# Performance work log

Measured on AMD Instinct MI355X. Metric: run time of the kernel, lower is better.

The kernel has to match this reference:

```python
import jax, jax.numpy as jnp
import numpy as np

# ---- constants from init_kwargs ----
L = 10.0
N = 512
DT = 5e-05
NUM_STEPS = 256
NUM_G = 4
DX = L / (N - 1)
DX2 = DX * DX
DT2 = DT * DT


def _wave_speed_map(alpha):
    # matches create_wave_speed_map: 2 + sum_i a_i * exp(-((x-cx_i)^2 + (y-cy_i)^2))
    x = jnp.linspace(-(L // 2), L // 2, N, dtype=jnp.float32)
    X, Y = jnp.meshgrid(x, x, indexing='ij')  # (N, N)
    amps = alpha[:NUM_G]
    cx = alpha[NUM_G:2 * NUM_G]
    cy = alpha[2 * NUM_G:3 * NUM_G]
    g = jnp.exp(-((X[None] - cx[:, None, None]) ** 2 + (Y[None] - cy[:, None, None]) ** 2))  # (G,N,N)
    return 2.0 + jnp.einsum('g,gij->ij', amps, g)


def setup_inputs() -> dict:
    key = jax.random.key(0)
    k1, k2 = jax.random.split(key)
    u0 = jax.random.normal(k1, (N, N), dtype=jnp.float32)
    alpha = jax.random.uniform(k2, (4 * NUM_G,), dtype=jnp.float32)
    return {"u0": u0, "alpha": alpha}


def reference(u0, alpha):
    c2_int = _wave_speed_map(alpha)[1:-1, 1:-1] ** 2  # (N-2, N-2)

    def step(carry, _):
        u, u_prev = carry
        u_xx = (u[:-2, 1:-1] - 2.0 * u[1:-1, 1:-1] + u[2:, 1:-1]) / DX2
        u_yy = (u[1:-1, :-2] - 2.0 * u[1:-1, 1:-1] + u[1:-1, 2:]) / DX2
        interior = 2.0 * u[1:-1, 1:-1] - u_prev[1:-1, 1:-1] + DT2 * c2_int * (u_xx + u_yy)
        # boundaries are zeroed every step in the original
        u_new = jnp.zeros_like(u).at[1:-1, 1:-1].set(interior)
        return (u_new, u), u  # record state BEFORE stepping, like intermediate_steps[t] = T

    (_, _), traj = jax.lax.scan(step, (u0, u0), None, length=NUM_STEPS)
    # original returns intermediate_steps[1:]
    return traj[1:]
```

## Files before the change

### kernel.cpp

```cpp
#include <hip/hip_runtime.h>

#define GN      512
#define GNN     (GN * GN)
#define TILE    32
#define HALO    16
#define REGW    64
#define LSTR    68
#define LROWS   66
#define NTHR    1024

__global__ __launch_bounds__(NTHR)
void wave_chunk(const float* __restrict__ ucur,
                const float* __restrict__ uprev,
                const float* __restrict__ alpha,
                float* __restrict__ out,
                int slice0, int nsteps)
{
    __shared__ __align__(16) float bufA[LROWS * LSTR];
    __shared__ __align__(16) float bufB[LROWS * LSTR];

    const int tid = threadIdx.x;
    const int r   = tid >> 4;
    const int c   = tid & 15;
    const int jc  = c << 2;

    const int bx  = blockIdx.x & 15;
    const int by  = blockIdx.x >> 4;
    const int ti0 = by * TILE, tj0 = bx * TILE;
    const int gi  = ti0 - HALO + r;
    const int gj0 = tj0 - HALO + jc;

    for (int k = tid; k < LROWS * LSTR; k += NTHR) { bufA[k] = 0.0f; bufB[k] = 0.0f; }

    const float DX = 10.0f / 511.0f;
    const float K  = (5e-5f * 5e-5f) / (DX * DX);

    float amp[4], cxs[4], cys[4];
#pragma unroll
    for (int g = 0; g < 4; ++g) {
        amp[g] = alpha[g];
        cxs[g] = alpha[4 + g];
        cys[g] = alpha[8 + g];
    }
    const float X = -5.0f + (float)gi * DX;
    float4 c2v;
    {
        float cm[4];
#pragma unroll
        for (int m = 0; m < 4; ++m) {
            const float Y = -5.0f + (float)(gj0 + m) * DX;
            float cv = 2.0f;
#pragma unroll
            for (int g = 0; g < 4; ++g) {
                const float dx = X - cxs[g], dy = Y - cys[g];
                cv += amp[g] * __expf(-(dx * dx + dy * dy));
            }
            cm[m] = cv * cv;
        }
        c2v = make_float4(cm[0], cm[1], cm[2], cm[3]);
    }

    const bool rin = (gi >= 1) && (gi <= GN - 2);
    float4 bm;
    bm.x = (rin && gj0 + 0 >= 1 && gj0 + 0 <= GN - 2) ? 1.0f : 0.0f;
    bm.y = (rin && gj0 + 1 >= 1 && gj0 + 1 <= GN - 2) ? 1.0f : 0.0f;
    bm.z = (rin && gj0 + 2 >= 1 && gj0 + 2 <= GN - 2) ? 1.0f : 0.0f;
    bm.w = (rin && gj0 + 3 >= 1 && gj0 + 3 <= GN - 2) ? 1.0f : 0.0f;

    float4 cur4 = make_float4(0.f, 0.f, 0.f, 0.f);
    float4 prv4 = cur4;
    const bool rowin = ((unsigned)gi < GN);
    const bool colin = ((unsigned)gj0 <= (GN - 4));
    if (rowin && colin) {
        const size_t g = (size_t)gi * GN + gj0;
        cur4 = *reinterpret_cast<const float4*>(ucur + g);
        prv4 = *reinterpret_cast<const float4*>(uprev + g);
    }

    const int idx = (r + 1) * LSTR + jc;
    *reinterpret_cast<float4*>(bufA + idx) = cur4;
    __syncthreads();

    const bool inTile = (r >= HALO) && (r < HALO + TILE) &&
                        (jc >= HALO) && (jc < HALO + TILE);

    float* A = bufA;
    float* B = bufB;
    for (int s = 0; s < nsteps; ++s) {
        const float4 up = *reinterpret_cast<const float4*>(A + idx - LSTR);
        const float4 dn = *reinterpret_cast<const float4*>(A + idx + LSTR);
        const float  lf = A[idx - 1];
        const float  rt = A[idx + 4];

        float4 nw;
        nw.x = bm.x * (2.0f * cur4.x - prv4.x + K * c2v.x * (up.x + dn.x + lf     + cur4.y - 4.0f * cur4.x));
        nw.y = bm.y * (2.0f * cur4.y - prv4.y + K * c2v.y * (up.y + dn.y + cur4.x + cur4.z - 4.0f * cur4.y));
        nw.z = bm.z * (2.0f * cur4.z - prv4.z + K * c2v.z * (up.z + dn.z + cur4.y + cur4.w - 4.0f * cur4.z));
        nw.w = bm.w * (2.0f * cur4.w - prv4.w + K * c2v.w * (up.w + dn.w + cur4.z + rt     - 4.0f * cur4.w));

        *reinterpret_cast<float4*>(B + idx) = nw;
        prv4 = cur4;
        cur4 = nw;

        if (inTile) {
            *reinterpret_cast<float4*>(out + (size_t)(slice0 + s) * GNN
                                           + (size_t)gi * GN + gj0) = nw;
        }

        __syncthreads();
        float* t = A; A = B; B = t;
    }
}

extern "C" void kernel_launch(void* const* d_in, const int* in_sizes, int n_in,
                              void* d_out, int out_size, void* d_ws, size_t ws_size,
                              hipStream_t stream)
{
    const float* u0    = (const float*)d_in[0];
    const float* alpha = (const float*)d_in[1];
    float*       out   = (float*)d_out;

    int base = 0;
    for (int k = 0; k < 16; ++k) {
        const int steps = (k < 15) ? 16 : 15;
        const float* uc = (k == 0) ? u0 : out + (size_t)(base - 1) * GNN;
        const float* up = (k == 0) ? u0 : out + (size_t)(base - 2) * GNN;
        wave_chunk<<<dim3(256), dim3(NTHR), 0, stream>>>(uc, up, alpha, out, base, steps);
        base += steps;
    }
}
```

Before: 401.3 us.

## Exchange column neighbors via DPP wave shifts and only edge rows via LDS

Remaps each wavefront to a 4-row by 64-column strip held in registers. Left and right neighbors now come from DPP wave-shift intrinsics instead of LDS. Only the top and bottom rows of each strip are exchanged through small LDS surfaces. This cuts LDS reads and writes per step. The step loop is also unrolled by two so the register ping-pong needs no copies, and the barrier becomes an explicit lgkmcnt wait plus s_barrier. The risks are that it relies on DPP wave-shift support and zero-fill at the wave edges, and that output stores are now scalar rather than float4.

```diff
diff --git a/kernel.cpp b/kernel.cpp
--- a/kernel.cpp
+++ b/kernel.cpp
@@ -4,10 +4,17 @@
 #define GNN     (GN * GN)
 #define TILE    32
 #define HALO    16
-#define REGW    64
-#define LSTR    68
-#define LROWS   66
 #define NTHR    1024
+#define SURF    (17 * 64)
+
+__device__ __forceinline__ float dpp_left(float x) {
+    return __int_as_float(__builtin_amdgcn_update_dpp(
+        0, __float_as_int(x), 0x130, 0xF, 0xF, true));
+}
+__device__ __forceinline__ float dpp_right(float x) {
+    return __int_as_float(__builtin_amdgcn_update_dpp(
+        0, __float_as_int(x), 0x138, 0xF, 0xF, true));
+}
 
 __global__ __launch_bounds__(NTHR)
 void wave_chunk(const float* __restrict__ ucur,
@@ -16,21 +23,22 @@
                 float* __restrict__ out,
                 int slice0, int nsteps)
 {
-    __shared__ __align__(16) float bufA[LROWS * LSTR];
-    __shared__ __align__(16) float bufB[LROWS * LSTR];
+    __shared__ __align__(16) float surf[4 * SURF];
+    float* const topA = surf;
+    float* const botA = surf + SURF;
+    float* const topB = surf + 2 * SURF;
+    float* const botB = surf + 3 * SURF;
 
     const int tid = threadIdx.x;
-    const int r   = tid >> 4;
-    const int c   = tid & 15;
-    const int jc  = c << 2;
+    const int w   = tid >> 6;
+    const int l   = tid & 63;
 
     const int bx  = blockIdx.x & 15;
     const int by  = blockIdx.x >> 4;
-    const int ti0 = by * TILE, tj0 = bx * TILE;
-    const int gi  = ti0 - HALO + r;
-    const int gj0 = tj0 - HALO + jc;
+    const int gi0 = by * TILE - HALO + 4 * w;
+    const int gj  = bx * TILE - HALO + l;
 
-    for (int k = tid; k < LROWS * LSTR; k += NTHR) { bufA[k] = 0.0f; bufB[k] = 0.0f; }
+    for (int k = tid; k < 4 * SURF; k += NTHR) surf[k] = 0.0f;
 
     const float DX = 10.0f / 511.0f;
     const float K  = (5e-5f * 5e-5f) / (DX * DX);
@@ -42,74 +50,71 @@
         cxs[g] = alpha[4 + g];
         cys[g] = alpha[8 + g];
     }
-    const float X = -5.0f + (float)gi * DX;
-    float4 c2v;
-    {
-        float cm[4];
+    const float Y = -5.0f + (float)gj * DX;
+    float dy2[4];
 #pragma unroll
-        for (int m = 0; m < 4; ++m) {
-            const float Y = -5.0f + (float)(gj0 + m) * DX;
-            float cv = 2.0f;
+    for (int g = 0; g < 4; ++g) { const float dy = Y - cys[g]; dy2[g] = dy * dy; }
+
+    float kc2[4], bm[4], cur[4], prv[4];
+    const bool colin = ((unsigned)gj < GN);
 #pragma unroll
-            for (int g = 0; g < 4; ++g) {
-                const float dx = X - cxs[g], dy = Y - cys[g];
-                cv += amp[g] * __expf(-(dx * dx + dy * dy));
-            }
-            cm[m] = cv * cv;
+    for (int k = 0; k < 4; ++k) {
+        const int gi = gi0 + k;
+        const float X = -5.0f + (float)gi * DX;
+        float cv = 2.0f;
+#pragma unroll
+        for (int g = 0; g < 4; ++g) {
+            const float dx = X - cxs[g];
+            cv += amp[g] * __expf(-(dx * dx + dy2[g]));
         }
-        c2v = make_float4(cm[0], cm[1], cm[2], cm[3]);
+        kc2[k] = K * (cv * cv);
+        bm[k]  = (gi >= 1 && gi <= GN - 2 && gj >= 1 && gj <= GN - 2) ? 1.0f : 0.0f;
+        const bool inb = colin && ((unsigned)gi < GN);
+        const long off = (long)gi * GN + gj;
+        cur[k] = inb ? ucur[off] : 0.0f;
+        prv[k] = inb ? uprev[off] : 0.0f;
     }
 
-    const bool rin = (gi >= 1) && (gi <= GN - 2);
-    float4 bm;
-    bm.x = (rin && gj0 + 0 >= 1 && gj0 + 0 <= GN - 2) ? 1.0f : 0.0f;
-    bm.y = (rin && gj0 + 1 >= 1 && gj0 + 1 <= GN - 2) ? 1.0f : 0.0f;
-    bm.z = (rin && gj0 + 2 >= 1 && gj0 + 2 <= GN - 2) ? 1.0f : 0.0f;
-    bm.w = (rin && gj0 + 3 >= 1 && gj0 + 3 <= GN - 2) ? 1.0f : 0.0f;
+    const int sTop = (w << 6) + l;
+    const int sBot = sTop + 64;
 
-    float4 cur4 = make_float4(0.f, 0.f, 0.f, 0.f);
-    float4 prv4 = cur4;
-    const bool rowin = ((unsigned)gi < GN);
-    const bool colin = ((unsigned)gj0 <= (GN - 4));
-    if (rowin && colin) {
-        const size_t g = (size_t)gi * GN + gj0;
-        cur4 = *reinterpret_cast<const float4*>(ucur + g);
-        prv4 = *reinterpret_cast<const float4*>(uprev + g);
-    }
-
-    const int idx = (r + 1) * LSTR + jc;
-    *reinterpret_cast<float4*>(bufA + idx) = cur4;
+    __syncthreads();
+    topA[sTop] = cur[0];
+    botA[sBot] = cur[3];
     __syncthreads();
 
-    const bool inTile = (r >= HALO) && (r < HALO + TILE) &&
-                        (jc >= HALO) && (jc < HALO + TILE);
+    const bool inTile = (w >= 4 && w < 12) && (l >= HALO) && (l < HALO + TILE);
+    float* op = out + ((long)slice0 * GNN + (long)gi0 * GN + gj);
 
-    float* A = bufA;
-    float* B = bufB;
-    for (int s = 0; s < nsteps; ++s) {
-        const float4 up = *reinterpret_cast<const float4*>(A + idx - LSTR);
-        const float4 dn = *reinterpret_cast<const float4*>(A + idx + LSTR);
-        const float  lf = A[idx - 1];
-        const float  rt = A[idx + 4];
+#define STEP(c, p, tRd, bRd, tWr, bWr)  do {                                          \
+        const float up0 = bRd[sTop];                                                  \
+        const float dn3 = tRd[sBot];                                                  \
+        const float lr0 = dpp_left(c[0]) + dpp_right(c[0]);                           \
+        const float lr3 = dpp_left(c[3]) + dpp_right(c[3]);                           \
+        const float n0 = bm[0] * (2.0f*c[0] - p[0] + kc2[0]*(up0 + c[1] + lr0 - 4.0f*c[0])); \
+        const float n3 = bm[3] * (2.0f*c[3] - p[3] + kc2[3]*(c[2] + dn3 + lr3 - 4.0f*c[3])); \
+        tWr[sTop] = n0;                                                               \
+        bWr[sBot] = n3;                                                               \
+        const float lr1 = dpp_left(c[1]) + dpp_right(c[1]);                           \
+        const float lr2 = dpp_left(c[2]) + dpp_right(c[2]);                           \
+        const float n1 = bm[1] * (2.0f*c[1] - p[1] + kc2[1]*(c[0] + c[2] + lr1 - 4.0f*c[1])); \
+        const float n2 = bm[2] * (2.0f*c[2] - p[2] + kc2[2]*(c[1] + c[3] + lr2 - 4.0f*c[2])); \
+        p[0] = n0; p[1] = n1; p[2] = n2; p[3] = n3;                                   \
+        if (inTile) { op[0] = n0; op[GN] = n1; op[2*GN] = n2; op[3*GN] = n3; }        \
+        op += GNN;                                                                    \
+        asm volatile("s_waitcnt lgkmcnt(0)" ::: "memory");                            \
+        __builtin_amdgcn_s_barrier();                                                 \
+    } while (0)
 
-        float4 nw;
-        nw.x = bm.x * (2.0f * cur4.x - prv4.x + K * c2v.x * (up.x + dn.x + lf     + cur4.y - 4.0f * cur4.x));
-        nw.y = bm.y * (2.0f * cur4.y - prv4.y + K * c2v.y * (up.y + dn.y + cur4.x + cur4.z - 4.0f * cur4.y));
-        nw.z = bm.z * (2.0f * cur4.z - prv4.z + K * c2v.z * (up.z + dn.z + cur4.y + cur4.w - 4.0f * cur4.z));
-        nw.w = bm.w * (2.0f * cur4.w - prv4.w + K * c2v.w * (up.w + dn.w + cur4.z + rt     - 4.0f * cur4.w));
-
-        *reinterpret_cast<float4*>(B + idx) = nw;
-        prv4 = cur4;
-        cur4 = nw;
-
-        if (inTile) {
-            *reinterpret_cast<float4*>(out + (size_t)(slice0 + s) * GNN
-                                           + (size_t)gi * GN + gj0) = nw;
-        }
-
-        __syncthreads();
-        float* t = A; A = B; B = t;
+    int s = 0;
+    for (; s + 2 <= nsteps; s += 2) {
+        STEP(cur, prv, topA, botA, topB, botB);
+        STEP(prv, cur, topB, botB, topA, botA);
     }
+    if (s < nsteps) {
+        STEP(cur, prv, topA, botA, topB, botB);
+    }
+#undef STEP
 }
 
 extern "C" void kernel_launch(void* const* d_in, const int* in_sizes, int n_in,
```

Result: faster. 364.0 us (-9.3%).
